# Kernel tuning notes

Measured on AMD Instinct MI355X. Metric: run time of the kernel, lower is better.

The kernel has to match this reference:

```python
import jax, jax.numpy as jnp
import numpy as np

HEADS = 4
DIM_HEAD = 32
SCALE = DIM_HEAD ** -0.5
EPS = 1e-12  # torch F.normalize default eps


def setup_inputs() -> dict:
    key = jax.random.key(0)
    k1, k2, k3 = jax.random.split(key, 3)
    dim, hidden = 64, HEADS * DIM_HEAD
    x = jax.random.normal(k1, (2, dim, 16, 16, 16), dtype=jnp.float32)
    g = jnp.ones((dim,), dtype=jnp.float32)
    w_qkv = jax.random.normal(k2, (3 * hidden, dim), dtype=jnp.float32) * 0.05
    w_out = jax.random.normal(k3, (dim, hidden), dtype=jnp.float32) * 0.05
    b_out = jnp.zeros((dim,), dtype=jnp.float32)
    return {"x": x, "g": g, "w_qkv": w_qkv, "w_out": w_out, "b_out": b_out}


def reference(x, g, w_qkv, w_out, b_out):
    b, c, h, w, d = x.shape
    n = h * w * d
    # RMSNorm: F.normalize(x, dim=1) * g * sqrt(c)
    norm = jnp.sqrt(jnp.sum(x * x, axis=1, keepdims=True))
    xn = x / jnp.maximum(norm, EPS) * g[None, :, None, None, None] * (c ** 0.5)
    # 1x1 conv3d == channel GEMM
    qkv = jnp.einsum('bcxyz,oc->boxyz', xn, w_qkv)  # [b, 3*hidden, h, w, d]
    hidden = HEADS * DIM_HEAD
    q, k, v = jnp.split(qkv, 3, axis=1)
    def to_heads(t):
        return t.reshape(b, HEADS, DIM_HEAD, n)  # b h c (x y z)
    q, k, v = to_heads(q), to_heads(k), to_heads(v)
    q = q * SCALE
    sim = jnp.einsum('bhdi,bhdj->bhij', q, k)  # [b, h, n, n]
    # FAITHFUL BUG REPRODUCTION: torch.Logsoftmax does not exist, so the
    # except branch always runs and attn = sim (no softmax applied).
    attn = sim
    out = jnp.einsum('bhij,bhdj->bhid', attn, v)  # [b, h, n, dim_head]
    # 'b h (x y z) d -> b (h d) x y z'
    out = out.transpose(0, 1, 3, 2).reshape(b, hidden, h, w, d)
    out = jnp.einsum('bcxyz,oc->boxyz', out, w_out) + b_out[None, :, None, None, None]
    return out + x
```

## Files before the change

### kernel.cpp

```cpp
#include <hip/hip_runtime.h>
#include <math.h>

#define B 2
#define C 64
#define N 4096
#define O3 384
#define HID 128
#define NH 4
#define DH 32
#define JC 128
#define NCH (N / JC)
#define PB 64

#define SCALE 0.17677669529663687f

__global__ __launch_bounds__(256) void k1_rmsnorm_qkv(
    const float* __restrict__ x, const float* __restrict__ g,
    const float* __restrict__ wqkv, float* __restrict__ qkv)
{
    __shared__ float xs[C][PB + 1];
    __shared__ float part[4][PB];
    __shared__ float scale_s[PB];
    __shared__ float gs[C];

    const int t = threadIdx.x;
    const int bx = blockIdx.x;
    const int ob = bx / 128;
    const int pblk = bx % 128;
    const int b = pblk >> 6;
    const int p0 = (pblk & 63) * PB;

    const float* xb = x + (size_t)b * C * N + p0;
    #pragma unroll
    for (int it = 0; it < 4; ++it) {
        int idx = t + it * 256;
        int row = idx >> 4, c4 = (idx & 15) * 4;
        float4 v4 = *(const float4*)(xb + (size_t)row * N + c4);
        xs[row][c4] = v4.x; xs[row][c4 + 1] = v4.y;
        xs[row][c4 + 2] = v4.z; xs[row][c4 + 3] = v4.w;
    }
    if (t < C) gs[t] = g[t];
    __syncthreads();

    {
        int p = t & 63, cg = t >> 6;
        float s = 0.f;
        #pragma unroll
        for (int c = 0; c < 16; ++c) { float v_ = xs[cg * 16 + c][p]; s += v_ * v_; }
        part[cg][p] = s;
    }
    __syncthreads();
    if (t < PB) {
        float ss = part[0][t] + part[1][t] + part[2][t] + part[3][t];
        scale_s[t] = 8.0f / fmaxf(sqrtf(ss), 1e-12f);
    }
    __syncthreads();
    #pragma unroll
    for (int it = 0; it < 16; ++it) {
        int idx = t + it * 256;
        int c = idx >> 6, p = idx & 63;
        xs[c][p] *= scale_s[p] * gs[c];
    }
    __syncthreads();

    const int p = t & 63;
    const int og = __builtin_amdgcn_readfirstlane(t >> 6);
    const int obase = ob * 32 + og * 8;
    float acc[8] = {0,0,0,0,0,0,0,0};
    #pragma unroll
    for (int c4 = 0; c4 < 16; ++c4) {
        const float xv0 = xs[c4 * 4 + 0][p];
        const float xv1 = xs[c4 * 4 + 1][p];
        const float xv2 = xs[c4 * 4 + 2][p];
        const float xv3 = xs[c4 * 4 + 3][p];
        #pragma unroll
        for (int k = 0; k < 8; ++k) {
            const float4 w4 = *(const float4*)(wqkv + (size_t)(obase + k) * C + c4 * 4);
            acc[k] += w4.x * xv0 + w4.y * xv1 + w4.z * xv2 + w4.w * xv3;
        }
    }
    const float qs = (obase < HID) ? SCALE : 1.0f;
    float* outb = qkv + (size_t)b * O3 * N + p0 + p;
    #pragma unroll
    for (int k = 0; k < 8; ++k)
        outb[(size_t)(obase + k) * N] = acc[k] * qs;
}

__global__ __launch_bounds__(256) void k2_kv_outer(
    const float* __restrict__ qkv, float* __restrict__ mpart)
{
    __shared__ float ks[DH][JC + 4];
    __shared__ float vs[DH][JC + 4];
    const int t = threadIdx.x;
    const int bx = blockIdx.x;
    const int b = bx / (NH * NCH);
    const int rem = bx % (NH * NCH);
    const int h = rem / NCH, ch = rem % NCH;
    const int j0 = ch * JC;

    const float* kb = qkv + (size_t)b * O3 * N + (size_t)(HID + h * DH) * N + j0;
    const float* vb = qkv + (size_t)b * O3 * N + (size_t)(2 * HID + h * DH) * N + j0;
    #pragma unroll
    for (int it = 0; it < 4; ++it) {
        int idx = t + it * 256;
        int row = idx >> 5, c4 = (idx & 31) * 4;
        *(float4*)&ks[row][c4] = *(const float4*)(kb + (size_t)row * N + c4);
        *(float4*)&vs[row][c4] = *(const float4*)(vb + (size_t)row * N + c4);
    }
    __syncthreads();

    const int e = t >> 3, d0 = (t & 7) * 4;
    float a0 = 0, a1 = 0, a2 = 0, a3 = 0;
    #pragma unroll 8
    for (int j4 = 0; j4 < JC / 4; ++j4) {
        const float4 kk = *(const float4*)&ks[e][j4 * 4];
        const float4 v0 = *(const float4*)&vs[d0 + 0][j4 * 4];
        const float4 v1 = *(const float4*)&vs[d0 + 1][j4 * 4];
        const float4 v2 = *(const float4*)&vs[d0 + 2][j4 * 4];
        const float4 v3 = *(const float4*)&vs[d0 + 3][j4 * 4];
        a0 += kk.x * v0.x + kk.y * v0.y + kk.z * v0.z + kk.w * v0.w;
        a1 += kk.x * v1.x + kk.y * v1.y + kk.z * v1.z + kk.w * v1.w;
        a2 += kk.x * v2.x + kk.y * v2.y + kk.z * v2.z + kk.w * v2.w;
        a3 += kk.x * v3.x + kk.y * v3.y + kk.z * v3.z + kk.w * v3.w;
    }
    ((float4*)(mpart + (size_t)((b * NH + h) * NCH + ch) * 1024))[t] =
        make_float4(a0, a1, a2, a3);
}

__global__ __launch_bounds__(256) void k2b_fold_u(
    const float* __restrict__ mpart, const float* __restrict__ wout,
    float* __restrict__ U)
{
    __shared__ float Ms[8][DH + 1];
    const int t = threadIdx.x;
    const int bx = blockIdx.x;
    const int eq = bx & 3;
    const int bh = bx >> 2;
    const int b = bh / NH, h = bh % NH;

    const float* mp = mpart + (size_t)bh * NCH * 1024 + eq * 256;
    float acc = 0.f;
    #pragma unroll 8
    for (int ch = 0; ch < NCH; ++ch)
        acc += mp[(size_t)ch * 1024 + t];
    Ms[t >> 5][t & 31] = acc;
    __syncthreads();

    #pragma unroll
    for (int half = 0; half < 2; ++half) {
        int u = t + half * 256;
        int o = u & 63, er = u >> 6;
        float s = 0.f;
        #pragma unroll
        for (int d4 = 0; d4 < 8; ++d4) {
            const float4 w4 = *(const float4*)(wout + (size_t)o * HID + h * DH + d4 * 4);
            s += w4.x * Ms[er][d4 * 4 + 0] + w4.y * Ms[er][d4 * 4 + 1]
               + w4.z * Ms[er][d4 * 4 + 2] + w4.w * Ms[er][d4 * 4 + 3];
        }
        U[((size_t)b * C + o) * HID + h * DH + eq * 8 + er] = s;
    }
}

__global__ __launch_bounds__(256) void k3_final(
    const float* __restrict__ qkv, const float* __restrict__ U,
    const float* __restrict__ bout, const float* __restrict__ x,
    float* __restrict__ out)
{
    __shared__ float qs[HID][PB + 1];
    const int t = threadIdx.x;
    const int bx = blockIdx.x;
    const int ob = bx / 128;
    const int pblk = bx % 128;
    const int b = pblk >> 6;
    const int p0 = (pblk & 63) * PB;

    const float* qb = qkv + (size_t)b * O3 * N + p0;
    #pragma unroll
    for (int it = 0; it < 8; ++it) {
        int idx = t + it * 256;
        int row = idx >> 4, c4 = (idx & 15) * 4;
        float4 v4 = *(const float4*)(qb + (size_t)row * N + c4);
        qs[row][c4] = v4.x; qs[row][c4 + 1] = v4.y;
        qs[row][c4 + 2] = v4.z; qs[row][c4 + 3] = v4.w;
    }
    __syncthreads();

    const int p = t & 63;
    const int og = __builtin_amdgcn_readfirstlane(t >> 6);
    const int o0 = ob * 16 + og * 4;
    const float* Ub = U + ((size_t)b * C + o0) * HID;
    float a0 = bout[o0], a1 = bout[o0 + 1], a2 = bout[o0 + 2], a3 = bout[o0 + 3];
    #pragma unroll
    for (int c4 = 0; c4 < 32; ++c4) {
        const float q0 = qs[c4 * 4 + 0][p];
        const float q1 = qs[c4 * 4 + 1][p];
        const float q2 = qs[c4 * 4 + 2][p];
        const float q3 = qs[c4 * 4 + 3][p];
        const float4 u0 = *(const float4*)(Ub + 0 * HID + c4 * 4);
        const float4 u1 = *(const float4*)(Ub + 1 * HID + c4 * 4);
        const float4 u2 = *(const float4*)(Ub + 2 * HID + c4 * 4);
        const float4 u3 = *(const float4*)(Ub + 3 * HID + c4 * 4);
        a0 += u0.x * q0 + u0.y * q1 + u0.z * q2 + u0.w * q3;
        a1 += u1.x * q0 + u1.y * q1 + u1.z * q2 + u1.w * q3;
        a2 += u2.x * q0 + u2.y * q1 + u2.z * q2 + u2.w * q3;
        a3 += u3.x * q0 + u3.y * q1 + u3.z * q2 + u3.w * q3;
    }
    const float* xb = x + ((size_t)b * C + o0) * N + p0 + p;
    float* ob_ = out + ((size_t)b * C + o0) * N + p0 + p;
    ob_[0 * N] = a0 + xb[0 * N];
    ob_[1 * N] = a1 + xb[1 * N];
    ob_[2 * N] = a2 + xb[2 * N];
    ob_[3 * N] = a3 + xb[3 * N];
}

extern "C" void kernel_launch(void* const* d_in, const int* in_sizes, int n_in,
                              void* d_out, int out_size, void* d_ws, size_t ws_size,
                              hipStream_t stream)
{
    const float* x    = (const float*)d_in[0];
    const float* g    = (const float*)d_in[1];
    const float* wqkv = (const float*)d_in[2];
    const float* wout = (const float*)d_in[3];
    const float* bout = (const float*)d_in[4];
    float* out = (float*)d_out;

    float* qkv   = (float*)d_ws;
    float* mpart = qkv + (size_t)B * O3 * N;
    float* U     = mpart + (size_t)B * NH * NCH * 1024;

    k1_rmsnorm_qkv<<<12 * 128, 256, 0, stream>>>(x, g, wqkv, qkv);
    k2_kv_outer<<<B * NH * NCH, 256, 0, stream>>>(qkv, mpart);
    k2b_fold_u<<<B * NH * 4, 256, 0, stream>>>(mpart, wout, U);
    k3_final<<<4 * 128, 256, 0, stream>>>(qkv, U, bout, x, out);
}
```

Measured before the change: 96.81 us.

## Split RMSNorm scale into separate kernel, halve KV chunk, double final-stage blocks

Adds a small kernel that computes the per-position RMSNorm scale once, so the QKV kernel no longer recomputes the norm and needs fewer syncs. The KV outer-product chunk shrinks from 128 to 64 positions, doubling the block count, and the final projection kernel uses twice as many blocks with two outputs per thread instead of four. Shared-memory loads are vectorized with padded rows. This trades an extra launch and more partial sums to fold for more parallelism across the GPU.

```diff
diff --git a/kernel.cpp b/kernel.cpp
--- a/kernel.cpp
+++ b/kernel.cpp
@@ -8,20 +8,34 @@
 #define HID 128
 #define NH 4
 #define DH 32
-#define JC 128
+#define JC 64
 #define NCH (N / JC)
 #define PB 64
 
 #define SCALE 0.17677669529663687f
 
-__global__ __launch_bounds__(256) void k1_rmsnorm_qkv(
+__global__ __launch_bounds__(128) void k0_scale(
+    const float* __restrict__ x, float* __restrict__ scale)
+{
+    const int bx = blockIdx.x;
+    const int b = bx >> 5;
+    const int p = (bx & 31) * 128 + threadIdx.x;
+    const float* xb = x + (size_t)b * C * N + p;
+    float s = 0.f;
+    #pragma unroll 8
+    for (int c = 0; c < C; ++c) {
+        float v = xb[(size_t)c * N];
+        s += v * v;
+    }
+    scale[(size_t)b * N + p] = 8.0f / fmaxf(sqrtf(s), 1e-12f);
+}
+
+__global__ __launch_bounds__(256) void k1_qkv(
     const float* __restrict__ x, const float* __restrict__ g,
-    const float* __restrict__ wqkv, float* __restrict__ qkv)
-{
-    __shared__ float xs[C][PB + 1];
-    __shared__ float part[4][PB];
-    __shared__ float scale_s[PB];
-    __shared__ float gs[C];
+    const float* __restrict__ scale, const float* __restrict__ wqkv,
+    float* __restrict__ qkv)
+{
+    __shared__ float xs[C][68];
 
     const int t = threadIdx.x;
     const int bx = blockIdx.x;
@@ -31,35 +45,18 @@
     const int p0 = (pblk & 63) * PB;
 
     const float* xb = x + (size_t)b * C * N + p0;
+    const float* scb = scale + (size_t)b * N + p0;
     #pragma unroll
     for (int it = 0; it < 4; ++it) {
         int idx = t + it * 256;
         int row = idx >> 4, c4 = (idx & 15) * 4;
         float4 v4 = *(const float4*)(xb + (size_t)row * N + c4);
-        xs[row][c4] = v4.x; xs[row][c4 + 1] = v4.y;
-        xs[row][c4 + 2] = v4.z; xs[row][c4 + 3] = v4.w;
-    }
-    if (t < C) gs[t] = g[t];
-    __syncthreads();
-
-    {
-        int p = t & 63, cg = t >> 6;
-        float s = 0.f;
-        #pragma unroll
-        for (int c = 0; c < 16; ++c) { float v_ = xs[cg * 16 + c][p]; s += v_ * v_; }
-        part[cg][p] = s;
-    }
-    __syncthreads();
-    if (t < PB) {
-        float ss = part[0][t] + part[1][t] + part[2][t] + part[3][t];
-        scale_s[t] = 8.0f / fmaxf(sqrtf(ss), 1e-12f);
-    }
-    __syncthreads();
-    #pragma unroll
-    for (int it = 0; it < 16; ++it) {
-        int idx = t + it * 256;
-        int c = idx >> 6, p = idx & 63;
-        xs[c][p] *= scale_s[p] * gs[c];
+        float4 s4 = *(const float4*)(scb + c4);
+        float gv = g[row];
+        xs[row][c4 + 0] = v4.x * gv * s4.x;
+        xs[row][c4 + 1] = v4.y * gv * s4.y;
+        xs[row][c4 + 2] = v4.z * gv * s4.z;
+        xs[row][c4 + 3] = v4.w * gv * s4.w;
     }
     __syncthreads();
 
@@ -101,9 +98,9 @@
     const float* kb = qkv + (size_t)b * O3 * N + (size_t)(HID + h * DH) * N + j0;
     const float* vb = qkv + (size_t)b * O3 * N + (size_t)(2 * HID + h * DH) * N + j0;
     #pragma unroll
-    for (int it = 0; it < 4; ++it) {
+    for (int it = 0; it < 2; ++it) {
         int idx = t + it * 256;
-        int row = idx >> 5, c4 = (idx & 31) * 4;
+        int row = idx >> 4, c4 = (idx & 15) * 4;
         *(float4*)&ks[row][c4] = *(const float4*)(kb + (size_t)row * N + c4);
         *(float4*)&vs[row][c4] = *(const float4*)(vb + (size_t)row * N + c4);
     }
@@ -111,7 +108,7 @@
 
     const int e = t >> 3, d0 = (t & 7) * 4;
     float a0 = 0, a1 = 0, a2 = 0, a3 = 0;
-    #pragma unroll 8
+    #pragma unroll
     for (int j4 = 0; j4 < JC / 4; ++j4) {
         const float4 kk = *(const float4*)&ks[e][j4 * 4];
         const float4 v0 = *(const float4*)&vs[d0 + 0][j4 * 4];
@@ -166,11 +163,11 @@
     const float* __restrict__ bout, const float* __restrict__ x,
     float* __restrict__ out)
 {
-    __shared__ float qs[HID][PB + 1];
-    const int t = threadIdx.x;
-    const int bx = blockIdx.x;
-    const int ob = bx / 128;
-    const int pblk = bx % 128;
+    __shared__ float qs[HID][68];
+    const int t = threadIdx.x;
+    const int bx = blockIdx.x;
+    const int ob = bx >> 7;
+    const int pblk = bx & 127;
     const int b = pblk >> 6;
     const int p0 = (pblk & 63) * PB;
 
@@ -179,17 +176,15 @@
     for (int it = 0; it < 8; ++it) {
         int idx = t + it * 256;
         int row = idx >> 4, c4 = (idx & 15) * 4;
-        float4 v4 = *(const float4*)(qb + (size_t)row * N + c4);
-        qs[row][c4] = v4.x; qs[row][c4 + 1] = v4.y;
-        qs[row][c4 + 2] = v4.z; qs[row][c4 + 3] = v4.w;
+        *(float4*)&qs[row][c4] = *(const float4*)(qb + (size_t)row * N + c4);
     }
     __syncthreads();
 
     const int p = t & 63;
     const int og = __builtin_amdgcn_readfirstlane(t >> 6);
-    const int o0 = ob * 16 + og * 4;
+    const int o0 = ob * 8 + og * 2;
     const float* Ub = U + ((size_t)b * C + o0) * HID;
-    float a0 = bout[o0], a1 = bout[o0 + 1], a2 = bout[o0 + 2], a3 = bout[o0 + 3];
+    float a0 = bout[o0], a1 = bout[o0 + 1];
     #pragma unroll
     for (int c4 = 0; c4 < 32; ++c4) {
         const float q0 = qs[c4 * 4 + 0][p];
@@ -198,19 +193,13 @@
         const float q3 = qs[c4 * 4 + 3][p];
         const float4 u0 = *(const float4*)(Ub + 0 * HID + c4 * 4);
         const float4 u1 = *(const float4*)(Ub + 1 * HID + c4 * 4);
-        const float4 u2 = *(const float4*)(Ub + 2 * HID + c4 * 4);
-        const float4 u3 = *(const float4*)(Ub + 3 * HID + c4 * 4);
         a0 += u0.x * q0 + u0.y * q1 + u0.z * q2 + u0.w * q3;
         a1 += u1.x * q0 + u1.y * q1 + u1.z * q2 + u1.w * q3;
-        a2 += u2.x * q0 + u2.y * q1 + u2.z * q2 + u2.w * q3;
-        a3 += u3.x * q0 + u3.y * q1 + u3.z * q2 + u3.w * q3;
     }
     const float* xb = x + ((size_t)b * C + o0) * N + p0 + p;
     float* ob_ = out + ((size_t)b * C + o0) * N + p0 + p;
-    ob_[0 * N] = a0 + xb[0 * N];
-    ob_[1 * N] = a1 + xb[1 * N];
-    ob_[2 * N] = a2 + xb[2 * N];
-    ob_[3 * N] = a3 + xb[3 * N];
+    ob_[0] = a0 + xb[0];
+    ob_[(size_t)N] = a1 + xb[(size_t)N];
 }
 
 extern "C" void kernel_launch(void* const* d_in, const int* in_sizes, int n_in,
@@ -227,9 +216,11 @@
     float* qkv   = (float*)d_ws;
     float* mpart = qkv + (size_t)B * O3 * N;
     float* U     = mpart + (size_t)B * NH * NCH * 1024;
-
-    k1_rmsnorm_qkv<<<12 * 128, 256, 0, stream>>>(x, g, wqkv, qkv);
+    float* scale = U + (size_t)B * C * HID;
+
+    k0_scale<<<64, 128, 0, stream>>>(x, scale);
+    k1_qkv<<<12 * 128, 256, 0, stream>>>(x, g, scale, wqkv, qkv);
     k2_kv_outer<<<B * NH * NCH, 256, 0, stream>>>(qkv, mpart);
     k2b_fold_u<<<B * NH * 4, 256, 0, stream>>>(mpart, wout, U);
-    k3_final<<<4 * 128, 256, 0, stream>>>(qkv, U, bout, x, out);
-}
+    k3_final<<<8 * 128, 256, 0, stream>>>(qkv, U, bout, x, out);
+}
```

New measurement: 100.2 us. 3.4% more time.
